# Performance work log

Hardware: AMD Instinct MI355X
Metric: run time of the kernel (lower is better)

Reference implementation:

```python
import jax, jax.numpy as jnp
import numpy as np

B, S, N, D, O = 64, 512, 128, 768, 3


def _xavier(k, shape):
    lim = (6.0 / (shape[0] + shape[1])) ** 0.5
    return jax.random.uniform(k, shape, jnp.float32, -lim, lim)


def setup_inputs() -> dict:
    key = jax.random.key(0)
    ks = jax.random.split(key, 16)
    sentence_embed = jax.random.normal(ks[0], (B, S, D), jnp.float32)
    # sparse binary dependency-graph adjacencies
    dg = (jax.random.uniform(ks[1], (B, N, N)) < 0.08).astype(jnp.float32)
    dg1 = (jax.random.uniform(ks[2], (B, N, N)) < 0.08).astype(jnp.float32)
    # target token span inside the sentence: [start, end), end > start
    start = jax.random.randint(ks[3], (B,), 1, 400)
    length = jax.random.randint(ks[4], (B,), 1, 16)
    target_span = jnp.stack([start, start + length], -1).astype(jnp.int32)
    # contiguous subword spans per GCN node (tran_indices), non-overlapping
    lens = jax.random.randint(ks[5], (B, N), 1, 4)
    ends = jnp.minimum(jnp.cumsum(lens, axis=1), S - 2)
    starts = jnp.concatenate([jnp.zeros((B, 1), ends.dtype), ends[:, :-1]], axis=1)
    tran_spans = jnp.stack([starts, ends], -1).astype(jnp.int32)  # [B,N,2]
    # node span of the target in the GCN graph (span_indices[i][0])
    gs = jax.random.randint(ks[6], (B,), 0, N - 8)
    gl = jax.random.randint(ks[7], (B,), 1, 8)
    gcn_span = jnp.stack([gs, gs + gl], -1).astype(jnp.int32)
    # parameters
    W_proj = _xavier(ks[8], (D, D))
    Wg1 = _xavier(ks[9], (D, D))
    Wg2 = _xavier(ks[10], (D, D))
    Wg3 = _xavier(ks[11], (D, D))
    stdv = 1.0 / np.sqrt(D)
    bg1 = jax.random.uniform(ks[12], (D,), jnp.float32, -stdv, stdv)
    bg2 = jax.random.uniform(ks[13], (D,), jnp.float32, -stdv, stdv)
    bg3 = jax.random.uniform(ks[14], (D,), jnp.float32, -stdv, stdv)
    fc_W = _xavier(ks[15], (2 * D, O))
    fc_b = jnp.zeros((O,), jnp.float32)
    return dict(sentence_embed=sentence_embed, dg=dg, dg1=dg1, W_proj=W_proj,
                Wg1=Wg1, bg1=bg1, Wg2=Wg2, bg2=bg2, Wg3=Wg3, bg3=bg3,
                fc_W=fc_W, fc_b=fc_b, target_span=target_span,
                tran_spans=tran_spans, gcn_span=gcn_span)


def reference(sentence_embed, dg, dg1, W_proj, Wg1, bg1, Wg2, bg2, Wg3, bg3,
              fc_W, fc_b, target_span, tran_spans, gcn_span):
    dt = sentence_embed.dtype
    pos = jnp.arange(S)
    # --- ragged target max-pool over sentence_embed[l:r] -> [B, D] ---
    tmask = (pos[None, :] >= target_span[:, 0:1]) & (pos[None, :] < target_span[:, 1:2])
    neg = jnp.finfo(dt).min
    target_max = jnp.max(jnp.where(tmask[:, :, None], sentence_embed, neg), axis=1)
    # --- ragged span-sum into GCN node features (tran_indices loop) -> [B, N, D] ---
    # torch slices [s+1 : e+1]
    nmask = ((pos[None, None, :] >= tran_spans[..., 0:1] + 1) &
             (pos[None, None, :] < tran_spans[..., 1:2] + 1)).astype(dt)  # [B,N,S]
    tmps = jnp.einsum('bns,bsd->bnd', nmask, sentence_embed)
    # --- GCN stack (GraphConvolution, bigcn=False) ---
    x = jax.nn.relu(tmps @ W_proj)
    adj = dg + dg1
    adj = jnp.where(adj >= 1, jnp.ones((), dt), adj)
    denom = jnp.sum(adj, axis=2, keepdims=True) + 1e-07
    def gcn(h, W, b):
        return jnp.einsum('bnm,bmd->bnd', adj, h @ W) / denom + b
    x = jax.nn.relu(gcn(x, Wg1, bg1)) + x
    x = jax.nn.relu(gcn(x, Wg2, bg2)) + x
    x = jax.nn.relu(gcn(x, Wg3, bg3)) + x
    # --- ragged node-span sum over GCN output -> [B, D] ---
    npos = jnp.arange(N)
    gmask = ((npos[None, :] >= gcn_span[:, 0:1]) & (npos[None, :] < gcn_span[:, 1:2])).astype(dt)
    gcn_target = jnp.einsum('bn,bnd->bd', gmask, x)
    # --- head ---
    logits = jnp.tanh(jnp.concatenate([target_max, gcn_target], axis=1) @ fc_W + fc_b)
    return logits
```

## Files before the change

### kernel.cpp

```cpp
#include <hip/hip_runtime.h>
#include <float.h>
#include <math.h>

typedef __attribute__((ext_vector_type(8))) short short8;
typedef __attribute__((ext_vector_type(4))) float f32x4;
typedef __attribute__((ext_vector_type(4))) unsigned short u16x4;
typedef unsigned short u16;
typedef unsigned int u32;

constexpr int B_ = 64, S_ = 512, N_ = 128, D_ = 768;

__device__ inline u16 f2h(float x) {
    _Float16 hh = (_Float16)x;
    return __builtin_bit_cast(u16, hh);
}
__device__ inline float h2f(u16 h) {
    return (float)__builtin_bit_cast(_Float16, h);
}

__device__ inline void gload_lds16(const u16* g, u16* s) {
    __builtin_amdgcn_global_load_lds(
        (const __attribute__((address_space(1))) u32*)g,
        (__attribute__((address_space(3))) u32*)s, 16, 0, 0);
}

__device__ inline int fragIdx(int row, int col) {
    return ((row >> 4) * 24 + (col >> 5)) * 512 + ((col >> 3) & 3) * 128
         + (row & 15) * 8 + (col & 7);
}

__global__ __launch_bounds__(192)
void span_split_kernel(const float* __restrict__ se, const int* __restrict__ spans,
                       u16* __restrict__ th) {
    const int bn = blockIdx.x;
    const int b  = bn >> 7;
    const int s  = spans[bn * 2 + 0];
    const int e  = spans[bn * 2 + 1];
    const float* base = se + (size_t)b * S_ * D_;
    const int d4 = threadIdx.x;
    float4 acc = make_float4(0.f, 0.f, 0.f, 0.f);
    for (int r = s + 1; r <= e; ++r) {
        const float4 v = reinterpret_cast<const float4*>(base + (size_t)r * D_)[d4];
        acc.x += v.x; acc.y += v.y; acc.z += v.z; acc.w += v.w;
    }
    u16x4 hv;
    hv[0] = f2h(acc.x); hv[1] = f2h(acc.y);
    hv[2] = f2h(acc.z); hv[3] = f2h(acc.w);
    *(u16x4*)(th + fragIdx(bn, d4 * 4)) = hv;
}

__global__ __launch_bounds__(192)
void target_max_kernel(const float* __restrict__ se, const int* __restrict__ tspan,
                       float* __restrict__ tmax) {
    const int b = blockIdx.x;
    const int c = blockIdx.y * 192 + threadIdx.x;
    const int s = tspan[b * 2 + 0];
    const int e = tspan[b * 2 + 1];
    const float* base = se + (size_t)b * S_ * D_ + c;
    float m = -FLT_MAX;
    for (int r = s; r < e; ++r) m = fmaxf(m, base[(size_t)r * D_]);
    tmax[(size_t)b * D_ + c] = m;
}

__global__ __launch_bounds__(128)
void adj_kernel(const float* __restrict__ dg, const float* __restrict__ dg1,
                u16* __restrict__ adj, float* __restrict__ invden) {
    const int row = blockIdx.x;
    const int t   = threadIdx.x;
    const size_t idx = (size_t)row * N_ + t;
    float a = dg[idx] + dg1[idx];
    a = (a >= 1.f) ? 1.f : a;
    adj[idx] = f2h(a);
    float w = a;
    #pragma unroll
    for (int off = 32; off; off >>= 1) w += __shfl_down(w, off, 64);
    __shared__ float ssum[2];
    if ((t & 63) == 0) ssum[t >> 6] = w;
    __syncthreads();
    if (t == 0) invden[row] = 1.f / (ssum[0] + ssum[1] + 1e-7f);
}

__global__ __launch_bounds__(256)
void wsplit_kernel(const float* __restrict__ W0, const float* __restrict__ W1,
                   const float* __restrict__ W2, const float* __restrict__ W3,
                   u16* __restrict__ wth) {
    __shared__ float t[64][65];
    const int mi = blockIdx.z;
    const float* W = (mi == 0) ? W0 : (mi == 1) ? W1 : (mi == 2) ? W2 : W3;
    const int k0 = blockIdx.y * 64, n0 = blockIdx.x * 64;
    #pragma unroll 4
    for (int it = 0; it < 16; ++it) {
        const int lin = it * 256 + threadIdx.x;
        const int r = lin >> 6, c = lin & 63;
        t[r][c] = W[(size_t)(k0 + r) * D_ + n0 + c];
    }
    __syncthreads();
    u16* oh = wth + (size_t)mi * D_ * D_;
    #pragma unroll 4
    for (int it = 0; it < 16; ++it) {
        const int lin = it * 256 + threadIdx.x;
        const int r = lin >> 6, c = lin & 63;
        oh[(size_t)(n0 + r) * D_ + k0 + c] = f2h(t[c][r]);
    }
}

template<int MODE>
__global__ __launch_bounds__(512, 4)
void gemm_fused(const u16* __restrict__ Ah,
                const u16* __restrict__ Bh,
                const u16* __restrict__ ADJ, const float* __restrict__ invden,
                const float* __restrict__ bias,
                u16* __restrict__ Oh) {
    __shared__ u16 lds[28672];
    const int tid  = threadIdx.x;
    const int lane = tid & 63, w = tid >> 6;
    const int wr = w >> 1, wc = w & 1;
    const int lr = lane & 15, lh = lane >> 4;

    int bid = blockIdx.x;
    bid = (bid & 7) * 64 + (bid >> 3);
    const int bnb = bid & 7, bmb = bid >> 3;
    const int bn = bnb * 96;

    const int qch = (lane & 3) ^ ((lane >> 3) & 3);
    const u16* gBsrc = Bh + (size_t)(bn + w * 16 + (lane >> 2)) * 768 + qch * 8;

    const int mblk0 = bmb * 8 + wr * 2;
    const u16* gAstage = Ah + (size_t)(bmb * 8 + w) * 12288 + lane * 8;

    f32x4 acc[2][3];
    #pragma unroll
    for (int i = 0; i < 2; ++i)
        #pragma unroll
        for (int j = 0; j < 3; ++j)
            acc[i][j] = (f32x4){0.f, 0.f, 0.f, 0.f};

    gload_lds16(gAstage,       lds + w * 1024);
    gload_lds16(gAstage + 512, lds + w * 1024 + 512);
    if (w < 6) {
        gload_lds16(gBsrc,      lds + 16384 + w * 512);
        gload_lds16(gBsrc + 32, lds + 16384 + 3072 + w * 512);
    }

    const int pB = (lh ^ ((lr >> 1) & 3)) << 3;

#define GEMM_ITER(C)                                                          \
    {                                                                         \
        const int t_ = 2 * tt + (C);                                          \
        asm volatile("s_waitcnt vmcnt(0)" ::: "memory");                      \
        __builtin_amdgcn_s_barrier();                                         \
        __builtin_amdgcn_sched_barrier(0);                                    \
        if (t_ <= 10) {                                                       \
            u16* ab = lds + (((C) + 1) & 1) * 8192;                           \
            gload_lds16(gAstage + (2 * (t_ + 1)) * 512,     ab + w * 1024);   \
            gload_lds16(gAstage + (2 * (t_ + 1) + 1) * 512, ab + w * 1024 + 512); \
            if (w < 6) {                                                      \
                u16* bb = lds + 16384 + (((C) + 1) & 1) * 6144;               \
                gload_lds16(gBsrc + (t_ + 1) * 64,      bb + w * 512);        \
                gload_lds16(gBsrc + (t_ + 1) * 64 + 32, bb + 3072 + w * 512); \
            }                                                                 \
        }                                                                     \
        const u16* La = lds + ((C) & 1) * 8192;                               \
        const u16* Lb = lds + 16384 + ((C) & 1) * 6144;                       \
        short8 aF[2][2], bF[3][2];                                            \
        _Pragma("unroll")                                                     \
        for (int sl = 0; sl < 2; ++sl) {                                      \
            aF[0][sl] = *(const short8*)&La[(wr * 2) * 1024 + sl * 512 + lane * 8];     \
            aF[1][sl] = *(const short8*)&La[(wr * 2 + 1) * 1024 + sl * 512 + lane * 8]; \
            _Pragma("unroll")                                                 \
            for (int f = 0; f < 3; ++f)                                       \
                bF[f][sl] = *(const short8*)&Lb[sl * 3072 + (wc * 48 + f * 16 + lr) * 32 + pB]; \
        }                                                                     \
        __builtin_amdgcn_s_setprio(1);                                        \
        _Pragma("unroll")                                                     \
        for (int sl = 0; sl < 2; ++sl)                                        \
            _Pragma("unroll")                                                 \
            for (int mf = 0; mf < 2; ++mf)                                    \
                _Pragma("unroll")                                             \
                for (int nf = 0; nf < 3; ++nf)                                \
                    acc[mf][nf] = __builtin_amdgcn_mfma_f32_16x16x32_f16(aF[mf][sl], bF[nf][sl], acc[mf][nf], 0, 0, 0); \
        __builtin_amdgcn_s_setprio(0);                                        \
    }

    for (int tt = 0; tt < 6; ++tt) {
        GEMM_ITER(0)
        GEMM_ITER(1)
    }
#undef GEMM_ITER

    if (MODE == 0) {
        #pragma unroll
        for (int mf = 0; mf < 2; ++mf) {
            const int mblk = mblk0 + mf;
            #pragma unroll
            for (int r = 0; r < 4; ++r) {
                const int lane_r = lh * 4 + r;
                #pragma unroll
                for (int nf = 0; nf < 3; ++nf) {
                    const int c = bn + wc * 48 + nf * 16 + lr;
                    const int idx = (mblk * 24 + (c >> 5)) * 512
                                  + ((c >> 3) & 3) * 128 + lane_r * 8 + (c & 7);
                    Oh[idx] = f2h(fmaxf(acc[mf][nf][r], 0.f));
                }
            }
        }
        return;
    }

    __builtin_amdgcn_s_barrier();
    __builtin_amdgcn_sched_barrier(0);

    const u16* adjb = ADJ + (size_t)bmb * (N_ * N_);
    short8 adjr[8];
    #pragma unroll
    for (int mf = 0; mf < 2; ++mf)
        #pragma unroll
        for (int ks = 0; ks < 4; ++ks)
            adjr[mf * 4 + ks] = *(const short8*)(adjb +
                (size_t)(wr * 32 + mf * 16 + lr) * 128 + ks * 32 + lh * 8);

    u16* hwT = lds;
    #pragma unroll
    for (int mf = 0; mf < 2; ++mf) {
        const int node0 = wr * 32 + mf * 16 + lh * 4;
        #pragma unroll
        for (int nf = 0; nf < 3; ++nf) {
            const int c = wc * 48 + nf * 16 + lr;
            u16x4 hv;
            #pragma unroll
            for (int r = 0; r < 4; ++r) hv[r] = f2h(acc[mf][nf][r]);
            *(u16x4*)&hwT[c * 128 + (((node0 >> 3) ^ (c & 7)) << 3) + (node0 & 7)] = hv;
        }
    }
    asm volatile("s_waitcnt lgkmcnt(0)" ::: "memory");
    __builtin_amdgcn_s_barrier();
    __builtin_amdgcn_sched_barrier(0);

    f32x4 acc2[2][3];
    #pragma unroll
    for (int i = 0; i < 2; ++i)
        #pragma unroll
        for (int j = 0; j < 3; ++j)
            acc2[i][j] = (f32x4){0.f, 0.f, 0.f, 0.f};

    #pragma unroll
    for (int ks = 0; ks < 4; ++ks) {
        short8 bf[3];
        #pragma unroll
        for (int f = 0; f < 3; ++f) {
            const int c = wc * 48 + f * 16 + lr;
            bf[f] = *(const short8*)&hwT[c * 128 + (((ks * 4 + lh) ^ (c & 7)) << 3)];
        }
        #pragma unroll
        for (int mf = 0; mf < 2; ++mf)
            #pragma unroll
            for (int nf = 0; nf < 3; ++nf)
                acc2[mf][nf] = __builtin_amdgcn_mfma_f32_16x16x32_f16(adjr[mf * 4 + ks], bf[nf], acc2[mf][nf], 0, 0, 0);
    }

    #pragma unroll
    for (int mf = 0; mf < 2; ++mf) {
        const int mblk = mblk0 + mf;
        #pragma unroll
        for (int r = 0; r < 4; ++r) {
            const int node = wr * 32 + mf * 16 + lh * 4 + r;
            const int lane_r = lh * 4 + r;
            const float inv = invden[bmb * N_ + node];
            #pragma unroll
            for (int nf = 0; nf < 3; ++nf) {
                const int c = bn + wc * 48 + nf * 16 + lr;
                const int idx = (mblk * 24 + (c >> 5)) * 512
                              + ((c >> 3) & 3) * 128 + lane_r * 8 + (c & 7);
                float v = fmaxf(acc2[mf][nf][r] * inv + bias[c], 0.f);
                v += h2f(Ah[idx]);
                Oh[idx] = f2h(v);
            }
        }
    }
}

__global__ __launch_bounds__(192)
void gcn_target_kernel(const u16* __restrict__ Xh,
                       const int* __restrict__ gspan, float* __restrict__ gt) {
    const int b = blockIdx.x;
    const int c = blockIdx.y * 192 + threadIdx.x;
    const int s = gspan[b * 2 + 0];
    const int e = gspan[b * 2 + 1];
    float acc = 0.f;
    for (int n = s; n < e; ++n)
        acc += h2f(Xh[fragIdx(b * N_ + n, c)]);
    gt[(size_t)b * D_ + c] = acc;
}

__global__ __launch_bounds__(256)
void head_kernel(const float* __restrict__ tmax, const float* __restrict__ gt,
                 const float* __restrict__ fcW, const float* __restrict__ fcb,
                 float* __restrict__ out) {
    const int b = blockIdx.x;
    const int t = threadIdx.x;
    float p0 = 0.f, p1 = 0.f, p2 = 0.f;
    for (int i = t; i < 2 * D_; i += 256) {
        const float v = (i < D_) ? tmax[(size_t)b * D_ + i] : gt[(size_t)b * D_ + i - D_];
        p0 += v * fcW[i * 3 + 0];
        p1 += v * fcW[i * 3 + 1];
        p2 += v * fcW[i * 3 + 2];
    }
    #pragma unroll
    for (int off = 32; off; off >>= 1) {
        p0 += __shfl_down(p0, off, 64);
        p1 += __shfl_down(p1, off, 64);
        p2 += __shfl_down(p2, off, 64);
    }
    __shared__ float red[4][3];
    const int wv = t >> 6;
    if ((t & 63) == 0) { red[wv][0] = p0; red[wv][1] = p1; red[wv][2] = p2; }
    __syncthreads();
    if (t == 0) {
        #pragma unroll
        for (int o = 0; o < 3; ++o) {
            const float s = red[0][o] + red[1][o] + red[2][o] + red[3][o] + fcb[o];
            out[b * 3 + o] = tanhf(s);
        }
    }
}

extern "C" void kernel_launch(void* const* d_in, const int* in_sizes, int n_in,
                              void* d_out, int out_size, void* d_ws, size_t ws_size,
                              hipStream_t stream) {
    const float* se   = (const float*)d_in[0];
    const float* dg   = (const float*)d_in[1];
    const float* dg1  = (const float*)d_in[2];
    const float* Wp   = (const float*)d_in[3];
    const float* Wg[3] = {(const float*)d_in[4], (const float*)d_in[6], (const float*)d_in[8]};
    const float* bg[3] = {(const float*)d_in[5], (const float*)d_in[7], (const float*)d_in[9]};
    const float* fcW  = (const float*)d_in[10];
    const float* fcb  = (const float*)d_in[11];
    const int*   tspan  = (const int*)d_in[12];
    const int*   nspans = (const int*)d_in[13];
    const int*   gspan  = (const int*)d_in[14];
    float* out = (float*)d_out;

    u16* us   = (u16*)d_ws;
    u16* X0   = us;
    u16* X1   = X0 + 6291456;
    u16* TH   = X1 + 6291456;
    u16* WTh  = TH + 6291456;
    u16* ADJ  = WTh + 2359296;
    float* INV = (float*)(ADJ + 1048576);
    float* TMX = INV + 8192;
    float* GT  = TMX + 49152;

    span_split_kernel<<<B_ * N_, 192, 0, stream>>>(se, nspans, TH);
    target_max_kernel<<<dim3(B_, 4), 192, 0, stream>>>(se, tspan, TMX);
    adj_kernel<<<B_ * N_, 128, 0, stream>>>(dg, dg1, ADJ, INV);
    wsplit_kernel<<<dim3(12, 12, 4), 256, 0, stream>>>(Wp, Wg[0], Wg[1], Wg[2], WTh);

    gemm_fused<0><<<512, 512, 0, stream>>>(TH, WTh,
                                           nullptr, nullptr, nullptr, X0);

    const u16* in_[3] = {X0, X1, X0};
    u16* out_[3] = {X1, X0, X1};
    for (int l = 0; l < 3; ++l) {
        const size_t wo = (size_t)(l + 1) * D_ * D_;
        gemm_fused<1><<<512, 512, 0, stream>>>(in_[l], WTh + wo,
                                               ADJ, INV, bg[l], out_[l]);
    }

    gcn_target_kernel<<<dim3(B_, 4), 192, 0, stream>>>(X1, gspan, GT);
    head_kernel<<<B_, 256, 0, stream>>>(TMX, GT, fcW, fcb, out);
}
```

Baseline: 108.7 us.

## Fuse gcn_target reduction into last GCN layer and target max into head

The final GCN layer gets a MODE 2 variant. Instead of writing the full node-feature tensor, it sums the in-span node rows per column in registers, reduces them across waves through LDS, and writes the per-batch target vector directly. The target-span max is moved into the head kernel, so two standalone kernels and the full last-layer output store go away. The costs are an extra LDS barrier in the last GEMM, and the head kernel now performs strided loads from the sentence embedding inside a serial per-block loop with only 64 blocks.

```diff
diff --git a/kernel.cpp b/kernel.cpp
--- a/kernel.cpp
+++ b/kernel.cpp
@@ -49,19 +49,6 @@
     *(u16x4*)(th + fragIdx(bn, d4 * 4)) = hv;
 }
 
-__global__ __launch_bounds__(192)
-void target_max_kernel(const float* __restrict__ se, const int* __restrict__ tspan,
-                       float* __restrict__ tmax) {
-    const int b = blockIdx.x;
-    const int c = blockIdx.y * 192 + threadIdx.x;
-    const int s = tspan[b * 2 + 0];
-    const int e = tspan[b * 2 + 1];
-    const float* base = se + (size_t)b * S_ * D_ + c;
-    float m = -FLT_MAX;
-    for (int r = s; r < e; ++r) m = fmaxf(m, base[(size_t)r * D_]);
-    tmax[(size_t)b * D_ + c] = m;
-}
-
 __global__ __launch_bounds__(128)
 void adj_kernel(const float* __restrict__ dg, const float* __restrict__ dg1,
                 u16* __restrict__ adj, float* __restrict__ invden) {
@@ -110,7 +97,8 @@
                 const u16* __restrict__ Bh,
                 const u16* __restrict__ ADJ, const float* __restrict__ invden,
                 const float* __restrict__ bias,
-                u16* __restrict__ Oh) {
+                u16* __restrict__ Oh,
+                const int* __restrict__ gspan, float* __restrict__ GT) {
     __shared__ u16 lds[28672];
     const int tid  = threadIdx.x;
     const int lane = tid & 63, w = tid >> 6;
@@ -258,6 +246,10 @@
                 acc2[mf][nf] = __builtin_amdgcn_mfma_f32_16x16x32_f16(adjr[mf * 4 + ks], bf[nf], acc2[mf][nf], 0, 0, 0);
     }
 
+    int gs = 0, ge = 0;
+    if (MODE == 2) { gs = gspan[bmb * 2 + 0]; ge = gspan[bmb * 2 + 1]; }
+    float pt[3] = {0.f, 0.f, 0.f};
+
     #pragma unroll
     for (int mf = 0; mf < 2; ++mf) {
         const int mblk = mblk0 + mf;
@@ -266,6 +258,7 @@
             const int node = wr * 32 + mf * 16 + lh * 4 + r;
             const int lane_r = lh * 4 + r;
             const float inv = invden[bmb * N_ + node];
+            const bool in_span = (node >= gs) && (node < ge);
             #pragma unroll
             for (int nf = 0; nf < 3; ++nf) {
                 const int c = bn + wc * 48 + nf * 16 + lr;
@@ -273,34 +266,51 @@
                               + ((c >> 3) & 3) * 128 + lane_r * 8 + (c & 7);
                 float v = fmaxf(acc2[mf][nf][r] * inv + bias[c], 0.f);
                 v += h2f(Ah[idx]);
-                Oh[idx] = f2h(v);
+                const u16 hv = f2h(v);
+                if (MODE == 1) Oh[idx] = hv;
+                else if (in_span) pt[nf] += h2f(hv);
             }
         }
     }
-}
-
-__global__ __launch_bounds__(192)
-void gcn_target_kernel(const u16* __restrict__ Xh,
-                       const int* __restrict__ gspan, float* __restrict__ gt) {
-    const int b = blockIdx.x;
-    const int c = blockIdx.y * 192 + threadIdx.x;
-    const int s = gspan[b * 2 + 0];
-    const int e = gspan[b * 2 + 1];
-    float acc = 0.f;
-    for (int n = s; n < e; ++n)
-        acc += h2f(Xh[fragIdx(b * N_ + n, c)]);
-    gt[(size_t)b * D_ + c] = acc;
+
+    if (MODE == 2) {
+        float* gtbuf = (float*)(lds + 16384);
+        const int contrib = wr * 4 + lh;
+        #pragma unroll
+        for (int nf = 0; nf < 3; ++nf)
+            gtbuf[(wc * 48 + nf * 16 + lr) * 16 + contrib] = pt[nf];
+        asm volatile("s_waitcnt lgkmcnt(0)" ::: "memory");
+        __builtin_amdgcn_s_barrier();
+        __builtin_amdgcn_sched_barrier(0);
+        if (tid < 96) {
+            float s = 0.f;
+            #pragma unroll
+            for (int i = 0; i < 16; ++i) s += gtbuf[tid * 16 + i];
+            GT[(size_t)bmb * D_ + bn + tid] = s;
+        }
+    }
 }
 
 __global__ __launch_bounds__(256)
-void head_kernel(const float* __restrict__ tmax, const float* __restrict__ gt,
+void head_kernel(const float* __restrict__ se, const int* __restrict__ tspan,
+                 const float* __restrict__ gt,
                  const float* __restrict__ fcW, const float* __restrict__ fcb,
                  float* __restrict__ out) {
     const int b = blockIdx.x;
     const int t = threadIdx.x;
+    const int s = tspan[b * 2 + 0];
+    const int e = tspan[b * 2 + 1];
     float p0 = 0.f, p1 = 0.f, p2 = 0.f;
     for (int i = t; i < 2 * D_; i += 256) {
-        const float v = (i < D_) ? tmax[(size_t)b * D_ + i] : gt[(size_t)b * D_ + i - D_];
+        float v;
+        if (i < D_) {
+            const float* base = se + (size_t)b * S_ * D_ + i;
+            float m = -FLT_MAX;
+            for (int r = s; r < e; ++r) m = fmaxf(m, base[(size_t)r * D_]);
+            v = m;
+        } else {
+            v = gt[(size_t)b * D_ + i - D_];
+        }
         p0 += v * fcW[i * 3 + 0];
         p1 += v * fcW[i * 3 + 1];
         p2 += v * fcW[i * 3 + 2];
@@ -318,8 +328,8 @@
     if (t == 0) {
         #pragma unroll
         for (int o = 0; o < 3; ++o) {
-            const float s = red[0][o] + red[1][o] + red[2][o] + red[3][o] + fcb[o];
-            out[b * 3 + o] = tanhf(s);
+            const float sacc = red[0][o] + red[1][o] + red[2][o] + red[3][o] + fcb[o];
+            out[b * 3 + o] = tanhf(sacc);
         }
     }
 }
@@ -347,25 +357,21 @@
     u16* WTh  = TH + 6291456;
     u16* ADJ  = WTh + 2359296;
     float* INV = (float*)(ADJ + 1048576);
-    float* TMX = INV + 8192;
-    float* GT  = TMX + 49152;
+    float* GT  = INV + 8192;
 
     span_split_kernel<<<B_ * N_, 192, 0, stream>>>(se, nspans, TH);
-    target_max_kernel<<<dim3(B_, 4), 192, 0, stream>>>(se, tspan, TMX);
     adj_kernel<<<B_ * N_, 128, 0, stream>>>(dg, dg1, ADJ, INV);
     wsplit_kernel<<<dim3(12, 12, 4), 256, 0, stream>>>(Wp, Wg[0], Wg[1], Wg[2], WTh);
 
-    gemm_fused<0><<<512, 512, 0, stream>>>(TH, WTh,
-                                           nullptr, nullptr, nullptr, X0);
-
-    const u16* in_[3] = {X0, X1, X0};
-    u16* out_[3] = {X1, X0, X1};
-    for (int l = 0; l < 3; ++l) {
-        const size_t wo = (size_t)(l + 1) * D_ * D_;
-        gemm_fused<1><<<512, 512, 0, stream>>>(in_[l], WTh + wo,
-                                               ADJ, INV, bg[l], out_[l]);
-    }
-
-    gcn_target_kernel<<<dim3(B_, 4), 192, 0, stream>>>(X1, gspan, GT);
-    head_kernel<<<B_, 256, 0, stream>>>(TMX, GT, fcW, fcb, out);
-}
+    gemm_fused<0><<<512, 512, 0, stream>>>(TH, WTh, nullptr, nullptr, nullptr,
+                                           X0, nullptr, nullptr);
+
+    gemm_fused<1><<<512, 512, 0, stream>>>(X0, WTh + (size_t)1 * D_ * D_,
+                                           ADJ, INV, bg[0], X1, nullptr, nullptr);
+    gemm_fused<1><<<512, 512, 0, stream>>>(X1, WTh + (size_t)2 * D_ * D_,
+                                           ADJ, INV, bg[1], X0, nullptr, nullptr);
+    gemm_fused<2><<<512, 512, 0, stream>>>(X0, WTh + (size_t)3 * D_ * D_,
+                                           ADJ, INV, bg[2], X1, gspan, GT);
+
+    head_kernel<<<B_, 256, 0, stream>>>(se, tspan, GT, fcW, fcb, out);
+}
```

After: 105.4 us. 1.03x faster.
